# Performance work log

Measured on AMD Instinct MI355X. Metric: run time of the kernel, lower is better.

Reference implementation:

```python
import jax, jax.numpy as jnp
import numpy as np


def setup_inputs() -> dict:
    key = jax.random.key(0)
    ks = jax.random.split(key, 5)
    B, Lq, Lkv, E, H = 4, 4096, 4096, 1024, 128
    x = jax.random.normal(ks[0], (B, Lq, E), dtype=jnp.float32)
    z = jax.random.normal(ks[1], (B, Lkv, E), dtype=jnp.float32)
    s = 1.0 / np.sqrt(E)
    Wq = jax.random.normal(ks[2], (H, E), dtype=jnp.float32) * s
    Wk = jax.random.normal(ks[3], (H, E), dtype=jnp.float32) * s
    Wv = jax.random.normal(ks[4], (H, E), dtype=jnp.float32) * s
    return {"x": x, "z": z, "Wq": Wq, "Wk": Wk, "Wv": Wv}


def reference(x, z, Wq, Wk, Wv):
    # q: [B, Lq, H]; k, v: [B, Lkv, H]  (torch Linear: y = x @ W.T)
    q = jnp.einsum('bqe,he->bqh', x, Wq)
    k = jnp.einsum('bke,he->bkh', z, Wk)
    v = jnp.einsum('bke,he->bkh', z, Wv)
    # NOTE: original code MULTIPLIES by sqrt(head_dim) (faithful reproduction)
    scale = jnp.asarray(k.shape[-1], x.dtype) ** 0.5
    weights = jnp.einsum('bqh,bkh->bqk', q, k) * scale  # [B, Lq, Lkv]
    weights = jax.nn.softmax(weights, axis=-1)
    logits = jnp.einsum('bqk,bkh->bqh', weights, v)  # [B, Lq, H]
    return logits
```

## Files before the change

kernel.cpp:

```cpp
#include <hip/hip_runtime.h>

typedef __attribute__((ext_vector_type(8))) short short8;
typedef __attribute__((ext_vector_type(4))) float f32x4;
typedef __attribute__((ext_vector_type(4))) float float4v;
typedef __attribute__((ext_vector_type(4))) unsigned short ushort4v;
typedef unsigned int __attribute__((may_alias)) u32ma;

#define B_   4
#define LQ   4096
#define LKV  4096
#define E_   1024
#define H_   128
#define NSPLIT 4
#define KVSPL (LKV / NSPLIT)
#define NT    (KVSPL / 64)
#define WELEM (H_ * E_)

static __device__ __forceinline__ unsigned short bf16_rne(float f) {
    unsigned int u = __float_as_uint(f);
    u += 0x7fffu + ((u >> 16) & 1u);
    return (unsigned short)(u >> 16);
}
static __device__ __forceinline__ float bf16_tof(unsigned short h) {
    return __uint_as_float(((unsigned int)h) << 16);
}
static __device__ __forceinline__ f32x4 mfma16(short8 a, short8 b, f32x4 c) {
    return __builtin_amdgcn_mfma_f32_16x16x32_bf16(a, b, c, 0, 0, 0);
}
static __device__ __forceinline__ void gload16(const unsigned short* g, unsigned short* l) {
    __builtin_amdgcn_global_load_lds(
        (const __attribute__((address_space(1))) unsigned int*)g,
        (__attribute__((address_space(3))) unsigned int*)l, 16, 0, 0);
}

__global__ __launch_bounds__(256) void convert_w_kernel(
    const float* __restrict__ Wq, const float* __restrict__ Wk, const float* __restrict__ Wv,
    unsigned short* __restrict__ wqh, unsigned short* __restrict__ wql,
    unsigned short* __restrict__ wkh, unsigned short* __restrict__ wkl,
    unsigned short* __restrict__ wvh)
{
    const int kb = blockIdx.x;
    const int which = blockIdx.y;
    const float* W = (which == 0) ? Wq : (which == 1) ? Wk : Wv;
    unsigned short* outh = (which == 0) ? wqh : (which == 1) ? wkh : wvh;
    unsigned short* outl = (which == 0) ? wql : wkl;
    const int t = threadIdx.x;
#pragma unroll
    for (int i = 0; i < 4; ++i) {
        const int c = t * 4 + i;
        const int h = c >> 3;
        const int k = kb * 64 + (((c & 7) ^ (h & 7)) * 8);
        const float* src = W + (size_t)h * E_ + k;
        float4v v0 = *(const float4v*)(src);
        float4v v1 = *(const float4v*)(src + 4);
        short8 hi, lo;
#pragma unroll
        for (int e = 0; e < 4; ++e) {
            unsigned short h0 = bf16_rne(v0[e]);
            unsigned short h1 = bf16_rne(v1[e]);
            hi[e] = (short)h0; hi[e + 4] = (short)h1;
            lo[e] = (short)bf16_rne(v0[e] - bf16_tof(h0));
            lo[e + 4] = (short)bf16_rne(v1[e] - bf16_tof(h1));
        }
        *(short8*)&outh[(size_t)kb * 8192 + (size_t)c * 8] = hi;
        if (which < 2) *(short8*)&outl[(size_t)kb * 8192 + (size_t)c * 8] = lo;
    }
}

__global__ __launch_bounds__(512, 1) void proj_kernel(
    const float* __restrict__ x, const float* __restrict__ z,
    const unsigned short* __restrict__ wqh, const unsigned short* __restrict__ wql,
    const unsigned short* __restrict__ wkh, const unsigned short* __restrict__ wkl,
    const unsigned short* __restrict__ wvh,
    unsigned short* __restrict__ qhi, unsigned short* __restrict__ qlo,
    unsigned short* __restrict__ khi, unsigned short* __restrict__ klo,
    unsigned short* __restrict__ vt)
{
    const int bid = blockIdx.x;
    const bool qmode = bid < 128;
    const int m0 = (qmode ? bid : bid - 128) * 128;
    const float* Asrc = qmode ? x : z;
    const unsigned short* W1h = qmode ? wqh : wkh;
    const unsigned short* W1l = qmode ? wql : wkl;

    const int t = threadIdx.x;
    const int w = t >> 6, l = t & 63, lg = (l >> 4) & 3, ll = l & 15;
    const int mw = w & 3, nw = w >> 2;

    __shared__ unsigned short Ah[8192];
    __shared__ unsigned short Al[8192];
    __shared__ unsigned short Wh[2][8192];
    __shared__ unsigned short Wl[2][8192];
    __shared__ unsigned short Wv2[2][8192];

    const int ar = t >> 2, aq = t & 3;
    float4v ra[4];
    auto loadA = [&](int e0) {
        const float* p = Asrc + (size_t)(m0 + ar) * E_ + e0 + aq * 16;
#pragma unroll
        for (int i = 0; i < 4; ++i) ra[i] = *(const float4v*)(p + i * 4);
    };
    auto writeA = [&]() {
#pragma unroll
        for (int half = 0; half < 2; ++half) {
            short8 hi, lo;
#pragma unroll
            for (int e = 0; e < 4; ++e) {
                float v0 = ra[2 * half][e];
                float v1 = ra[2 * half + 1][e];
                unsigned short h0 = bf16_rne(v0);
                unsigned short h1 = bf16_rne(v1);
                hi[e] = (short)h0; hi[e + 4] = (short)h1;
                lo[e] = (short)bf16_rne(v0 - bf16_tof(h0));
                lo[e + 4] = (short)bf16_rne(v1 - bf16_tof(h1));
            }
            const int j = 2 * aq + half;
            const int off = ar * 64 + ((j ^ (ar & 7)) * 8);
            *(short8*)&Ah[off] = hi;
            *(short8*)&Al[off] = lo;
        }
    };
    auto issueW = [&](int kb, int bsel) {
#pragma unroll
        for (int i = 0; i < 2; ++i) {
            const int cbase = w * 128 + i * 64;
            const size_t so = (size_t)kb * 8192 + (size_t)(cbase + l) * 8;
            gload16(W1h + so, &Wh[bsel][(size_t)cbase * 8]);
            gload16(W1l + so, &Wl[bsel][(size_t)cbase * 8]);
            if (!qmode) gload16(wvh + so, &Wv2[bsel][(size_t)cbase * 8]);
        }
    };

    f32x4 acc[2][4], accv[2][4];
    const f32x4 zz = {0.f, 0.f, 0.f, 0.f};
#pragma unroll
    for (int rf = 0; rf < 2; ++rf)
#pragma unroll
        for (int cf = 0; cf < 4; ++cf) { acc[rf][cf] = zz; accv[rf][cf] = zz; }

    issueW(0, 0);
    loadA(0);
    writeA();
    __syncthreads();

    for (int kb = 0; kb < 16; ++kb) {
        const int bsel = kb & 1;
        if (kb < 15) { issueW(kb + 1, bsel ^ 1); loadA((kb + 1) * 64); }

#pragma unroll
        for (int ks = 0; ks < 2; ++ks) {
            short8 a_h[2], a_l[2];
#pragma unroll
            for (int rf = 0; rf < 2; ++rf) {
                const int r = mw * 32 + rf * 16 + ll;
                const int off = r * 64 + (((ks * 4 + lg) ^ (ll & 7)) * 8);
                a_h[rf] = *(const short8*)&Ah[off];
                a_l[rf] = *(const short8*)&Al[off];
            }
#pragma unroll
            for (int cf = 0; cf < 4; ++cf) {
                const int hrow = nw * 64 + cf * 16 + ll;
                const int off = hrow * 64 + (((ks * 4 + lg) ^ (ll & 7)) * 8);
                short8 bh = *(const short8*)&Wh[bsel][off];
                short8 bl = *(const short8*)&Wl[bsel][off];
#pragma unroll
                for (int rf = 0; rf < 2; ++rf) {
                    acc[rf][cf] = mfma16(a_h[rf], bh, acc[rf][cf]);
                    acc[rf][cf] = mfma16(a_h[rf], bl, acc[rf][cf]);
                    acc[rf][cf] = mfma16(a_l[rf], bh, acc[rf][cf]);
                }
                if (!qmode) {
                    short8 bv = *(const short8*)&Wv2[bsel][off];
#pragma unroll
                    for (int rf = 0; rf < 2; ++rf)
                        accv[rf][cf] = mfma16(a_h[rf], bv, accv[rf][cf]);
                }
            }
        }
        __syncthreads();
        if (kb < 15) {
            writeA();
            __syncthreads();
        }
    }

#pragma unroll
    for (int rf = 0; rf < 2; ++rf)
#pragma unroll
        for (int cf = 0; cf < 4; ++cf)
#pragma unroll
            for (int j = 0; j < 4; ++j) {
                const int m = m0 + mw * 32 + rf * 16 + 4 * lg + j;
                const int h = nw * 64 + cf * 16 + ll;
                const float val = acc[rf][cf][j];
                unsigned short hi = bf16_rne(val);
                unsigned short lo = bf16_rne(val - bf16_tof(hi));
                const size_t o = (size_t)m * H_ + h;
                if (qmode) {
                    qhi[o] = hi; qlo[o] = lo;
                } else {
                    khi[o] = hi; klo[o] = lo;
                    const int b = m >> 12, kv = m & 4095;
                    vt[(size_t)b * ((size_t)H_ * LKV) + (size_t)h * LKV + kv] =
                        bf16_rne(accv[rf][cf][j]);
                }
            }
}

__global__ __launch_bounds__(512, 2) void attn_kernel(
    const unsigned short* __restrict__ qhi, const unsigned short* __restrict__ qlo,
    const unsigned short* __restrict__ khi, const unsigned short* __restrict__ klo,
    const unsigned short* __restrict__ vt,
    float* __restrict__ Opart, float* __restrict__ msb, float* __restrict__ lsb)
{
    const int blk = blockIdx.x;
    const int bb = blk & 3;
    const int qt = (blk >> 2) & 15;
    const int split = blk >> 6;
    const int t = threadIdx.x;
    const int w = t >> 6, l = t & 63, lg = (l >> 4) & 3, ll = l & 15;

    __shared__ unsigned short KT[2][24576];
    __shared__ unsigned short Pl[8][32][64];

    const float CSC = 11.313708498984761f * 1.4426950408889634f;

    short8 qh[2][4], ql[2][4];
#pragma unroll
    for (int b = 0; b < 2; ++b) {
        const size_t qrow = (size_t)(bb * LQ + qt * 256 + w * 32 + b * 16 + ll) * H_;
#pragma unroll
        for (int ks = 0; ks < 4; ++ks) {
            qh[b][ks] = *(const short8*)(qhi + qrow + ks * 32 + lg * 8);
            ql[b][ks] = *(const short8*)(qlo + qrow + ks * 32 + lg * 8);
        }
    }

    const int kv_base = split * KVSPL;

    auto issue_loads = [&](int kv0, int bsel) {
        unsigned short* base = &KT[bsel][0];
#pragma unroll
        for (int ci = 0; ci < 2; ++ci) {
            const int chunk = w * 2 + ci;
            {
                int row = chunk * 4 + (l >> 4);
                int c = l & 15;
                const unsigned short* src = khi + (size_t)(bb * LKV + kv0 + row) * H_
                                          + ((c ^ (row & 7)) * 8);
                gload16(src, base + chunk * 512);
            }
            {
                int row = chunk * 4 + (l >> 4);
                int c = l & 15;
                const unsigned short* src = klo + (size_t)(bb * LKV + kv0 + row) * H_
                                          + ((c ^ (row & 7)) * 8);
                gload16(src, base + 8192 + chunk * 512);
            }
            {
                int row = chunk * 8 + (l >> 3);
                int c = l & 7;
                const unsigned short* src = vt + (size_t)bb * ((size_t)H_ * LKV)
                                          + (size_t)row * LKV + kv0 + ((c ^ (row & 7)) * 8);
                gload16(src, base + 16384 + chunk * 512);
            }
        }
    };

    f32x4 O[8][2];
    const f32x4 zz = {0.f, 0.f, 0.f, 0.f};
#pragma unroll
    for (int f = 0; f < 8; ++f) { O[f][0] = zz; O[f][1] = zz; }
    float mold[2] = {-1e30f, -1e30f};
    float lsum[2] = {0.f, 0.f};

    issue_loads(kv_base, 0);
    __syncthreads();

    for (int ti = 0; ti < NT; ++ti) {
        const int bsel = ti & 1;
        if (ti + 1 < NT) issue_loads(kv_base + (ti + 1) * 64, bsel ^ 1);

        const unsigned short* Kb = &KT[bsel][0];

        f32x4 S[4][2];
#pragma unroll
        for (int a = 0; a < 4; ++a) { S[a][0] = zz; S[a][1] = zz; }
#pragma unroll
        for (int ks = 0; ks < 4; ++ks) {
#pragma unroll
            for (int a = 0; a < 4; ++a) {
                const int row = a * 16 + ll;
                const int off = row * 128 + (((ks * 4 + lg) ^ (ll & 7)) * 8);
                short8 kh = *(const short8*)(Kb + off);
                short8 kl2 = *(const short8*)(Kb + 8192 + off);
                S[a][0] = mfma16(kh, qh[0][ks], S[a][0]);
                S[a][0] = mfma16(kh, ql[0][ks], S[a][0]);
                S[a][0] = mfma16(kl2, qh[0][ks], S[a][0]);
                S[a][1] = mfma16(kh, qh[1][ks], S[a][1]);
                S[a][1] = mfma16(kh, ql[1][ks], S[a][1]);
                S[a][1] = mfma16(kl2, qh[1][ks], S[a][1]);
            }
        }

        float crr[2];
#pragma unroll
        for (int b = 0; b < 2; ++b) {
            float mx = S[0][b][0];
#pragma unroll
            for (int a = 0; a < 4; ++a)
#pragma unroll
                for (int j = 0; j < 4; ++j) mx = fmaxf(mx, S[a][b][j]);
            mx = fmaxf(mx, __shfl_xor(mx, 16));
            mx = fmaxf(mx, __shfl_xor(mx, 32));
            float mn = fmaxf(mold[b], mx * CSC);
            float corr = exp2f(mold[b] - mn);
            float ps = 0.f;
#pragma unroll
            for (int a = 0; a < 4; ++a) {
                float p0 = exp2f(fmaf(S[a][b][0], CSC, -mn));
                float p1 = exp2f(fmaf(S[a][b][1], CSC, -mn));
                float p2 = exp2f(fmaf(S[a][b][2], CSC, -mn));
                float p3 = exp2f(fmaf(S[a][b][3], CSC, -mn));
                ps += (p0 + p1) + (p2 + p3);
                unsigned int pk0, pk1;
                asm("v_cvt_pk_bf16_f32 %0, %1, %2" : "=v"(pk0) : "v"(p0), "v"(p1));
                asm("v_cvt_pk_bf16_f32 %0, %1, %2" : "=v"(pk1) : "v"(p2), "v"(p3));
                const int row = b * 16 + ll;
                u32ma* pd = (u32ma*)&Pl[w][0][0];
                const int di = row * 32 + (((2 * a + (lg >> 1)) ^ (ll & 7)) * 4) + 2 * (lg & 1);
                pd[di] = pk0;
                pd[di + 1] = pk1;
            }
            ps += __shfl_xor(ps, 16);
            ps += __shfl_xor(ps, 32);
            lsum[b] = lsum[b] * corr + ps;
            mold[b] = mn;
            crr[b] = corr;
        }
#pragma unroll
        for (int f = 0; f < 8; ++f) {
            O[f][0] *= crr[0];
            O[f][1] *= crr[1];
        }

        asm volatile("s_waitcnt lgkmcnt(0)" ::: "memory");
        __builtin_amdgcn_sched_barrier(0);

#pragma unroll
        for (int ks = 0; ks < 2; ++ks) {
            short8 pb[2];
#pragma unroll
            for (int b = 0; b < 2; ++b) {
                const int row = b * 16 + ll;
                pb[b] = *(const short8*)&Pl[w][row][((ks * 4 + lg) ^ (ll & 7)) * 8];
            }
#pragma unroll
            for (int f = 0; f < 8; ++f) {
                const int row = f * 16 + ll;
                short8 va = *(const short8*)(Kb + 16384 + row * 64
                                             + (((ks * 4 + lg) ^ (ll & 7)) * 8));
                O[f][0] = mfma16(va, pb[0], O[f][0]);
                O[f][1] = mfma16(va, pb[1], O[f][1]);
            }
        }

        __syncthreads();
    }

    const size_t obase = ((((size_t)split * 4 + bb) * 16 + qt) * 8 + w) * 16;
#pragma unroll
    for (int f = 0; f < 8; ++f)
#pragma unroll
        for (int b = 0; b < 2; ++b)
            *(float4v*)&Opart[(obase + f * 2 + b) * 256 + l * 4] = O[f][b];

    if (lg == 0) {
#pragma unroll
        for (int b = 0; b < 2; ++b) {
            const int q = qt * 256 + w * 32 + b * 16 + ll;
            msb[((size_t)split * 4 + bb) * LQ + q] = mold[b];
            lsb[((size_t)split * 4 + bb) * LQ + q] = lsum[b];
        }
    }
}

__global__ __launch_bounds__(512) void combine_kernel(
    const float* __restrict__ Opart, const float* __restrict__ msb,
    const float* __restrict__ lsb, float* __restrict__ out)
{
    const int blk = blockIdx.x;
    const int bb = blk & 3;
    const int qt = (blk >> 2) & 15;
    const int fg = blk >> 6;
    const int t = threadIdx.x;
    const int w = t >> 6, l = t & 63, lg = (l >> 4) & 3, ll = l & 15;

#pragma unroll
    for (int b = 0; b < 2; ++b) {
        const int q = qt * 256 + w * 32 + b * 16 + ll;
        float ms[NSPLIT], ls[NSPLIT];
#pragma unroll
        for (int s = 0; s < NSPLIT; ++s) {
            ms[s] = msb[((size_t)s * 4 + bb) * LQ + q];
            ls[s] = lsb[((size_t)s * 4 + bb) * LQ + q];
        }
        float mM = fmaxf(fmaxf(ms[0], ms[1]), fmaxf(ms[2], ms[3]));
        float wsp[NSPLIT];
        float L = 0.f;
#pragma unroll
        for (int s = 0; s < NSPLIT; ++s) {
            wsp[s] = exp2f(ms[s] - mM);
            L += ls[s] * wsp[s];
        }
        const float inv = 1.f / L;
#pragma unroll
        for (int fi = 0; fi < 2; ++fi) {
            const int f = fg * 2 + fi;
            f32x4 acc = {0.f, 0.f, 0.f, 0.f};
#pragma unroll
            for (int s = 0; s < NSPLIT; ++s) {
                const size_t ob = ((((size_t)s * 4 + bb) * 16 + qt) * 8 + w) * 16 + f * 2 + b;
                float4v ov = *(const float4v*)&Opart[ob * 256 + l * 4];
#pragma unroll
                for (int j = 0; j < 4; ++j) acc[j] += ov[j] * wsp[s];
            }
#pragma unroll
            for (int j = 0; j < 4; ++j) acc[j] *= inv;
            *(float4v*)&out[((size_t)bb * LQ + q) * H_ + f * 16 + lg * 4] = acc;
        }
    }
}

extern "C" void kernel_launch(void* const* d_in, const int* in_sizes, int n_in,
                              void* d_out, int out_size, void* d_ws, size_t ws_size,
                              hipStream_t stream) {
    const float* x  = (const float*)d_in[0];
    const float* z  = (const float*)d_in[1];
    const float* Wq = (const float*)d_in[2];
    const float* Wk = (const float*)d_in[3];
    const float* Wv = (const float*)d_in[4];
    float* out = (float*)d_out;

    const size_t NQ = (size_t)B_ * LQ * H_;
    unsigned short* qhi = (unsigned short*)d_ws;
    unsigned short* qlo = qhi + NQ;
    unsigned short* khi = qlo + NQ;
    unsigned short* klo = khi + NQ;
    unsigned short* vtp = klo + NQ;
    float* Opart = (float*)(vtp + NQ);
    float* msb   = Opart + (size_t)NSPLIT * NQ;
    float* lsb   = msb + (size_t)NSPLIT * B_ * LQ;
    unsigned short* wqh = (unsigned short*)(lsb + (size_t)NSPLIT * B_ * LQ);
    unsigned short* wql = wqh + WELEM;
    unsigned short* wkh = wql + WELEM;
    unsigned short* wkl = wkh + WELEM;
    unsigned short* wvh = wkl + WELEM;

    convert_w_kernel<<<dim3(16, 3), 256, 0, stream>>>(Wq, Wk, Wv, wqh, wql, wkh, wkl, wvh);
    proj_kernel<<<dim3(256), 512, 0, stream>>>(x, z, wqh, wql, wkh, wkl, wvh,
                                               qhi, qlo, khi, klo, vtp);
    attn_kernel<<<dim3(256), 512, 0, stream>>>(qhi, qlo, khi, klo, vtp, Opart, msb, lsb);
    combine_kernel<<<dim3(256), 512, 0, stream>>>(Opart, msb, lsb, out);
}
```

Baseline: 141.0 us.

## Halve attention query tile per wave, shrink LDS, and split K/V staging

Each wave now processes 16 query rows instead of 32, so the attention grid doubles to 512 blocks and the launch-bounds occupancy hint rises from 2 to 4 blocks per CU. K hi/lo are now single-buffered and reloaded after a mid-iteration barrier, while V stays double-buffered, which cuts LDS per block. The aim is better latency hiding through more resident waves and more blocks across the CUs. In exchange, each K tile loaded from global memory and LDS now feeds half as many MFMAs, and each iteration adds an extra barrier and a full vmcnt wait. The combine kernel is remapped to the new Opart layout.

```diff
diff --git a/kernel.cpp b/kernel.cpp
--- a/kernel.cpp
+++ b/kernel.cpp
@@ -207,7 +207,7 @@
             }
 }
 
-__global__ __launch_bounds__(512, 2) void attn_kernel(
+__global__ __launch_bounds__(512, 4) void attn_kernel(
     const unsigned short* __restrict__ qhi, const unsigned short* __restrict__ qlo,
     const unsigned short* __restrict__ khi, const unsigned short* __restrict__ klo,
     const unsigned short* __restrict__ vt,
@@ -215,173 +215,154 @@
 {
     const int blk = blockIdx.x;
     const int bb = blk & 3;
-    const int qt = (blk >> 2) & 15;
-    const int split = blk >> 6;
+    const int qt = (blk >> 2) & 31;
+    const int split = blk >> 7;
     const int t = threadIdx.x;
     const int w = t >> 6, l = t & 63, lg = (l >> 4) & 3, ll = l & 15;
 
-    __shared__ unsigned short KT[2][24576];
-    __shared__ unsigned short Pl[8][32][64];
+    __shared__ unsigned short Kh[8192];
+    __shared__ unsigned short Kl[8192];
+    __shared__ unsigned short Vb[2][8192];
+    __shared__ unsigned short Pl[8][16][64];
 
     const float CSC = 11.313708498984761f * 1.4426950408889634f;
 
-    short8 qh[2][4], ql[2][4];
-#pragma unroll
-    for (int b = 0; b < 2; ++b) {
-        const size_t qrow = (size_t)(bb * LQ + qt * 256 + w * 32 + b * 16 + ll) * H_;
+    short8 qh[4], ql[4];
+    {
+        const size_t qrow = (size_t)(bb * LQ + qt * 128 + w * 16 + ll) * H_;
 #pragma unroll
         for (int ks = 0; ks < 4; ++ks) {
-            qh[b][ks] = *(const short8*)(qhi + qrow + ks * 32 + lg * 8);
-            ql[b][ks] = *(const short8*)(qlo + qrow + ks * 32 + lg * 8);
+            qh[ks] = *(const short8*)(qhi + qrow + ks * 32 + lg * 8);
+            ql[ks] = *(const short8*)(qlo + qrow + ks * 32 + lg * 8);
         }
     }
 
     const int kv_base = split * KVSPL;
-
-    auto issue_loads = [&](int kv0, int bsel) {
-        unsigned short* base = &KT[bsel][0];
+    const unsigned short* khb = khi + (size_t)bb * LKV * H_;
+    const unsigned short* klb = klo + (size_t)bb * LKV * H_;
+    const unsigned short* vbg = vt + (size_t)bb * ((size_t)H_ * LKV);
+
+    auto issue_K = [&](int kv0) {
 #pragma unroll
         for (int ci = 0; ci < 2; ++ci) {
             const int chunk = w * 2 + ci;
-            {
-                int row = chunk * 4 + (l >> 4);
-                int c = l & 15;
-                const unsigned short* src = khi + (size_t)(bb * LKV + kv0 + row) * H_
-                                          + ((c ^ (row & 7)) * 8);
-                gload16(src, base + chunk * 512);
-            }
-            {
-                int row = chunk * 4 + (l >> 4);
-                int c = l & 15;
-                const unsigned short* src = klo + (size_t)(bb * LKV + kv0 + row) * H_
-                                          + ((c ^ (row & 7)) * 8);
-                gload16(src, base + 8192 + chunk * 512);
-            }
-            {
-                int row = chunk * 8 + (l >> 3);
-                int c = l & 7;
-                const unsigned short* src = vt + (size_t)bb * ((size_t)H_ * LKV)
-                                          + (size_t)row * LKV + kv0 + ((c ^ (row & 7)) * 8);
-                gload16(src, base + 16384 + chunk * 512);
-            }
+            const int row = chunk * 4 + (l >> 4);
+            const int c = l & 15;
+            const size_t so = (size_t)(kv0 + row) * H_ + ((c ^ (row & 7)) * 8);
+            gload16(khb + so, &Kh[chunk * 512]);
+            gload16(klb + so, &Kl[chunk * 512]);
         }
     };
-
-    f32x4 O[8][2];
+    auto issue_V = [&](int kv0, int bs) {
+#pragma unroll
+        for (int ci = 0; ci < 2; ++ci) {
+            const int chunk = w * 2 + ci;
+            const int row = chunk * 8 + (l >> 3);
+            const int c = l & 7;
+            gload16(vbg + (size_t)row * LKV + kv0 + ((c ^ (row & 7)) * 8),
+                    &Vb[bs][chunk * 512]);
+        }
+    };
+
+    f32x4 O[8];
     const f32x4 zz = {0.f, 0.f, 0.f, 0.f};
 #pragma unroll
-    for (int f = 0; f < 8; ++f) { O[f][0] = zz; O[f][1] = zz; }
-    float mold[2] = {-1e30f, -1e30f};
-    float lsum[2] = {0.f, 0.f};
-
-    issue_loads(kv_base, 0);
-    __syncthreads();
-
+    for (int f = 0; f < 8; ++f) O[f] = zz;
+    float mold = -1e30f;
+    float lsum = 0.f;
+
+    issue_K(kv_base);
+    issue_V(kv_base, 0);
+    asm volatile("s_waitcnt vmcnt(0)" ::: "memory");
+    __builtin_amdgcn_s_barrier();
+
+    int vsel = 0;
     for (int ti = 0; ti < NT; ++ti) {
-        const int bsel = ti & 1;
-        if (ti + 1 < NT) issue_loads(kv_base + (ti + 1) * 64, bsel ^ 1);
-
-        const unsigned short* Kb = &KT[bsel][0];
-
-        f32x4 S[4][2];
-#pragma unroll
-        for (int a = 0; a < 4; ++a) { S[a][0] = zz; S[a][1] = zz; }
+        if (ti + 1 < NT) issue_V(kv_base + (ti + 1) * 64, vsel ^ 1);
+        __builtin_amdgcn_sched_barrier(0);
+
+        f32x4 S[4];
+#pragma unroll
+        for (int a = 0; a < 4; ++a) S[a] = zz;
 #pragma unroll
         for (int ks = 0; ks < 4; ++ks) {
 #pragma unroll
             for (int a = 0; a < 4; ++a) {
                 const int row = a * 16 + ll;
                 const int off = row * 128 + (((ks * 4 + lg) ^ (ll & 7)) * 8);
-                short8 kh = *(const short8*)(Kb + off);
-                short8 kl2 = *(const short8*)(Kb + 8192 + off);
-                S[a][0] = mfma16(kh, qh[0][ks], S[a][0]);
-                S[a][0] = mfma16(kh, ql[0][ks], S[a][0]);
-                S[a][0] = mfma16(kl2, qh[0][ks], S[a][0]);
-                S[a][1] = mfma16(kh, qh[1][ks], S[a][1]);
-                S[a][1] = mfma16(kh, ql[1][ks], S[a][1]);
-                S[a][1] = mfma16(kl2, qh[1][ks], S[a][1]);
-            }
-        }
-
-        float crr[2];
-#pragma unroll
-        for (int b = 0; b < 2; ++b) {
-            float mx = S[0][b][0];
-#pragma unroll
-            for (int a = 0; a < 4; ++a)
-#pragma unroll
-                for (int j = 0; j < 4; ++j) mx = fmaxf(mx, S[a][b][j]);
-            mx = fmaxf(mx, __shfl_xor(mx, 16));
-            mx = fmaxf(mx, __shfl_xor(mx, 32));
-            float mn = fmaxf(mold[b], mx * CSC);
-            float corr = exp2f(mold[b] - mn);
-            float ps = 0.f;
-#pragma unroll
-            for (int a = 0; a < 4; ++a) {
-                float p0 = exp2f(fmaf(S[a][b][0], CSC, -mn));
-                float p1 = exp2f(fmaf(S[a][b][1], CSC, -mn));
-                float p2 = exp2f(fmaf(S[a][b][2], CSC, -mn));
-                float p3 = exp2f(fmaf(S[a][b][3], CSC, -mn));
-                ps += (p0 + p1) + (p2 + p3);
-                unsigned int pk0, pk1;
-                asm("v_cvt_pk_bf16_f32 %0, %1, %2" : "=v"(pk0) : "v"(p0), "v"(p1));
-                asm("v_cvt_pk_bf16_f32 %0, %1, %2" : "=v"(pk1) : "v"(p2), "v"(p3));
-                const int row = b * 16 + ll;
-                u32ma* pd = (u32ma*)&Pl[w][0][0];
-                const int di = row * 32 + (((2 * a + (lg >> 1)) ^ (ll & 7)) * 4) + 2 * (lg & 1);
-                pd[di] = pk0;
-                pd[di + 1] = pk1;
-            }
-            ps += __shfl_xor(ps, 16);
-            ps += __shfl_xor(ps, 32);
-            lsum[b] = lsum[b] * corr + ps;
-            mold[b] = mn;
-            crr[b] = corr;
-        }
-#pragma unroll
-        for (int f = 0; f < 8; ++f) {
-            O[f][0] *= crr[0];
-            O[f][1] *= crr[1];
-        }
+                short8 kh  = *(const short8*)&Kh[off];
+                short8 kl2 = *(const short8*)&Kl[off];
+                S[a] = mfma16(kh,  qh[ks], S[a]);
+                S[a] = mfma16(kh,  ql[ks], S[a]);
+                S[a] = mfma16(kl2, qh[ks], S[a]);
+            }
+        }
+
+        float mx = S[0][0];
+#pragma unroll
+        for (int a = 0; a < 4; ++a)
+#pragma unroll
+            for (int j = 0; j < 4; ++j) mx = fmaxf(mx, S[a][j]);
+        mx = fmaxf(mx, __shfl_xor(mx, 16));
+        mx = fmaxf(mx, __shfl_xor(mx, 32));
+        const float mn = fmaxf(mold, mx * CSC);
+        const float corr = exp2f(mold - mn);
+        float ps = 0.f;
+#pragma unroll
+        for (int a = 0; a < 4; ++a) {
+            float p0 = exp2f(fmaf(S[a][0], CSC, -mn));
+            float p1 = exp2f(fmaf(S[a][1], CSC, -mn));
+            float p2 = exp2f(fmaf(S[a][2], CSC, -mn));
+            float p3 = exp2f(fmaf(S[a][3], CSC, -mn));
+            ps += (p0 + p1) + (p2 + p3);
+            unsigned int pk0, pk1;
+            asm("v_cvt_pk_bf16_f32 %0, %1, %2" : "=v"(pk0) : "v"(p0), "v"(p1));
+            asm("v_cvt_pk_bf16_f32 %0, %1, %2" : "=v"(pk1) : "v"(p2), "v"(p3));
+            u32ma* pd = (u32ma*)&Pl[w][0][0];
+            const int di = ll * 32 + (((2 * a + (lg >> 1)) ^ (ll & 7)) * 4) + 2 * (lg & 1);
+            pd[di] = pk0;
+            pd[di + 1] = pk1;
+        }
+        ps += __shfl_xor(ps, 16);
+        ps += __shfl_xor(ps, 32);
+        lsum = lsum * corr + ps;
+        mold = mn;
+#pragma unroll
+        for (int f = 0; f < 8; ++f) O[f] *= corr;
 
         asm volatile("s_waitcnt lgkmcnt(0)" ::: "memory");
         __builtin_amdgcn_sched_barrier(0);
+        __builtin_amdgcn_s_barrier();
+        if (ti + 1 < NT) issue_K(kv_base + (ti + 1) * 64);
+        __builtin_amdgcn_sched_barrier(0);
 
 #pragma unroll
         for (int ks = 0; ks < 2; ++ks) {
-            short8 pb[2];
-#pragma unroll
-            for (int b = 0; b < 2; ++b) {
-                const int row = b * 16 + ll;
-                pb[b] = *(const short8*)&Pl[w][row][((ks * 4 + lg) ^ (ll & 7)) * 8];
-            }
+            short8 pb = *(const short8*)&Pl[w][ll][((ks * 4 + lg) ^ (ll & 7)) * 8];
 #pragma unroll
             for (int f = 0; f < 8; ++f) {
                 const int row = f * 16 + ll;
-                short8 va = *(const short8*)(Kb + 16384 + row * 64
-                                             + (((ks * 4 + lg) ^ (ll & 7)) * 8));
-                O[f][0] = mfma16(va, pb[0], O[f][0]);
-                O[f][1] = mfma16(va, pb[1], O[f][1]);
-            }
-        }
-
-        __syncthreads();
-    }
-
-    const size_t obase = ((((size_t)split * 4 + bb) * 16 + qt) * 8 + w) * 16;
+                short8 va = *(const short8*)&Vb[vsel][row * 64
+                                                     + (((ks * 4 + lg) ^ (ll & 7)) * 8)];
+                O[f] = mfma16(va, pb, O[f]);
+            }
+        }
+
+        asm volatile("s_waitcnt vmcnt(0)" ::: "memory");
+        __builtin_amdgcn_sched_barrier(0);
+        __builtin_amdgcn_s_barrier();
+        vsel ^= 1;
+    }
+
+    const size_t ob = (((size_t)split * 4 + bb) * 32 + qt) * 8 + w;
 #pragma unroll
     for (int f = 0; f < 8; ++f)
-#pragma unroll
-        for (int b = 0; b < 2; ++b)
-            *(float4v*)&Opart[(obase + f * 2 + b) * 256 + l * 4] = O[f][b];
+        *(float4v*)&Opart[(ob * 8 + f) * 256 + l * 4] = O[f];
 
     if (lg == 0) {
-#pragma unroll
-        for (int b = 0; b < 2; ++b) {
-            const int q = qt * 256 + w * 32 + b * 16 + ll;
-            msb[((size_t)split * 4 + bb) * LQ + q] = mold[b];
-            lsb[((size_t)split * 4 + bb) * LQ + q] = lsum[b];
-        }
+        const int q = qt * 128 + w * 16 + ll;
+        msb[((size_t)split * 4 + bb) * LQ + q] = mold;
+        lsb[((size_t)split * 4 + bb) * LQ + q] = lsum;
     }
 }
 
@@ -391,44 +372,41 @@
 {
     const int blk = blockIdx.x;
     const int bb = blk & 3;
-    const int qt = (blk >> 2) & 15;
-    const int fg = blk >> 6;
+    const int qt = (blk >> 2) & 31;
+    const int fg = blk >> 7;
     const int t = threadIdx.x;
     const int w = t >> 6, l = t & 63, lg = (l >> 4) & 3, ll = l & 15;
 
-#pragma unroll
-    for (int b = 0; b < 2; ++b) {
-        const int q = qt * 256 + w * 32 + b * 16 + ll;
-        float ms[NSPLIT], ls[NSPLIT];
+    const int q = qt * 128 + w * 16 + ll;
+    float ms[NSPLIT], ls[NSPLIT];
+#pragma unroll
+    for (int s = 0; s < NSPLIT; ++s) {
+        ms[s] = msb[((size_t)s * 4 + bb) * LQ + q];
+        ls[s] = lsb[((size_t)s * 4 + bb) * LQ + q];
+    }
+    float mM = fmaxf(fmaxf(ms[0], ms[1]), fmaxf(ms[2], ms[3]));
+    float wsp[NSPLIT];
+    float L = 0.f;
+#pragma unroll
+    for (int s = 0; s < NSPLIT; ++s) {
+        wsp[s] = exp2f(ms[s] - mM);
+        L += ls[s] * wsp[s];
+    }
+    const float inv = 1.f / L;
+#pragma unroll
+    for (int fi = 0; fi < 4; ++fi) {
+        const int f = fg * 4 + fi;
+        f32x4 acc = {0.f, 0.f, 0.f, 0.f};
 #pragma unroll
         for (int s = 0; s < NSPLIT; ++s) {
-            ms[s] = msb[((size_t)s * 4 + bb) * LQ + q];
-            ls[s] = lsb[((size_t)s * 4 + bb) * LQ + q];
-        }
-        float mM = fmaxf(fmaxf(ms[0], ms[1]), fmaxf(ms[2], ms[3]));
-        float wsp[NSPLIT];
-        float L = 0.f;
-#pragma unroll
-        for (int s = 0; s < NSPLIT; ++s) {
-            wsp[s] = exp2f(ms[s] - mM);
-            L += ls[s] * wsp[s];
-        }
-        const float inv = 1.f / L;
-#pragma unroll
-        for (int fi = 0; fi < 2; ++fi) {
-            const int f = fg * 2 + fi;
-            f32x4 acc = {0.f, 0.f, 0.f, 0.f};
-#pragma unroll
-            for (int s = 0; s < NSPLIT; ++s) {
-                const size_t ob = ((((size_t)s * 4 + bb) * 16 + qt) * 8 + w) * 16 + f * 2 + b;
-                float4v ov = *(const float4v*)&Opart[ob * 256 + l * 4];
-#pragma unroll
-                for (int j = 0; j < 4; ++j) acc[j] += ov[j] * wsp[s];
-            }
-#pragma unroll
-            for (int j = 0; j < 4; ++j) acc[j] *= inv;
-            *(float4v*)&out[((size_t)bb * LQ + q) * H_ + f * 16 + lg * 4] = acc;
-        }
+            const size_t ob = (((size_t)s * 4 + bb) * 32 + qt) * 8 + w;
+            float4v ov = *(const float4v*)&Opart[(ob * 8 + f) * 256 + l * 4];
+#pragma unroll
+            for (int j = 0; j < 4; ++j) acc[j] += ov[j] * wsp[s];
+        }
+#pragma unroll
+        for (int j = 0; j < 4; ++j) acc[j] *= inv;
+        *(float4v*)&out[((size_t)bb * LQ + q) * H_ + f * 16 + lg * 4] = acc;
     }
 }
 
@@ -460,6 +438,6 @@
     convert_w_kernel<<<dim3(16, 3), 256, 0, stream>>>(Wq, Wk, Wv, wqh, wql, wkh, wkl, wvh);
     proj_kernel<<<dim3(256), 512, 0, stream>>>(x, z, wqh, wql, wkh, wkl, wvh,
                                                qhi, qlo, khi, klo, vtp);
-    attn_kernel<<<dim3(256), 512, 0, stream>>>(qhi, qlo, khi, klo, vtp, Opart, msb, lsb);
+    attn_kernel<<<dim3(512), 512, 0, stream>>>(qhi, qlo, khi, klo, vtp, Opart, msb, lsb);
     combine_kernel<<<dim3(256), 512, 0, stream>>>(Opart, msb, lsb, out);
 }
```

Result: no change. 141.0 us (+0.0%).

## Split KV eight ways, single-buffer K/V in LDS, raise occupancy

Applied to the files above, without the earlier changes.

Templates the attention and combine kernels on the number of KV splits and uses eight splits (512 blocks) when the workspace is large enough. The double-buffered combined K/V LDS tile is replaced by separate single K and V buffers. Their reloads are staggered: K is reloaded after QK^T and V after PV, separated by barriers. The LDS saving allows launch bounds of 4 blocks per CU, and setprio is raised around the MFMA sections. The trade-off is more partial outputs to combine and less prefetch slack in exchange for more resident blocks to hide latency.

```diff
diff --git a/kernel.cpp b/kernel.cpp
--- a/kernel.cpp
+++ b/kernel.cpp
@@ -11,9 +11,6 @@
 #define LKV  4096
 #define E_   1024
 #define H_   128
-#define NSPLIT 4
-#define KVSPL (LKV / NSPLIT)
-#define NT    (KVSPL / 64)
 #define WELEM (H_ * E_)
 
 static __device__ __forceinline__ unsigned short bf16_rne(float f) {
@@ -207,12 +204,15 @@
             }
 }
 
-__global__ __launch_bounds__(512, 2) void attn_kernel(
+template<int NS>
+__global__ __launch_bounds__(512, 4) void attn_kernel(
     const unsigned short* __restrict__ qhi, const unsigned short* __restrict__ qlo,
     const unsigned short* __restrict__ khi, const unsigned short* __restrict__ klo,
     const unsigned short* __restrict__ vt,
     float* __restrict__ Opart, float* __restrict__ msb, float* __restrict__ lsb)
 {
+    constexpr int KVS = LKV / NS;
+    constexpr int NT  = KVS / 64;
     const int blk = blockIdx.x;
     const int bb = blk & 3;
     const int qt = (blk >> 2) & 15;
@@ -220,7 +220,9 @@
     const int t = threadIdx.x;
     const int w = t >> 6, l = t & 63, lg = (l >> 4) & 3, ll = l & 15;
 
-    __shared__ unsigned short KT[2][24576];
+    __shared__ unsigned short Kh[8192];
+    __shared__ unsigned short Kl[8192];
+    __shared__ unsigned short Vb[8192];
     __shared__ unsigned short Pl[8][32][64];
 
     const float CSC = 11.313708498984761f * 1.4426950408889634f;
@@ -236,34 +238,30 @@
         }
     }
 
-    const int kv_base = split * KVSPL;
-
-    auto issue_loads = [&](int kv0, int bsel) {
-        unsigned short* base = &KT[bsel][0];
+    const int kv_base = split * KVS;
+    const unsigned short* khb = khi + (size_t)bb * LKV * H_;
+    const unsigned short* klb = klo + (size_t)bb * LKV * H_;
+    const unsigned short* vbg = vt + (size_t)bb * ((size_t)H_ * LKV);
+
+    auto issue_K = [&](int kv0) {
 #pragma unroll
         for (int ci = 0; ci < 2; ++ci) {
             const int chunk = w * 2 + ci;
-            {
-                int row = chunk * 4 + (l >> 4);
-                int c = l & 15;
-                const unsigned short* src = khi + (size_t)(bb * LKV + kv0 + row) * H_
-                                          + ((c ^ (row & 7)) * 8);
-                gload16(src, base + chunk * 512);
-            }
-            {
-                int row = chunk * 4 + (l >> 4);
-                int c = l & 15;
-                const unsigned short* src = klo + (size_t)(bb * LKV + kv0 + row) * H_
-                                          + ((c ^ (row & 7)) * 8);
-                gload16(src, base + 8192 + chunk * 512);
-            }
-            {
-                int row = chunk * 8 + (l >> 3);
-                int c = l & 7;
-                const unsigned short* src = vt + (size_t)bb * ((size_t)H_ * LKV)
-                                          + (size_t)row * LKV + kv0 + ((c ^ (row & 7)) * 8);
-                gload16(src, base + 16384 + chunk * 512);
-            }
+            const int row = chunk * 4 + (l >> 4);
+            const int c = l & 15;
+            const size_t so = (size_t)(kv0 + row) * H_ + ((c ^ (row & 7)) * 8);
+            gload16(khb + so, &Kh[chunk * 512]);
+            gload16(klb + so, &Kl[chunk * 512]);
+        }
+    };
+    auto issue_V = [&](int kv0) {
+#pragma unroll
+        for (int ci = 0; ci < 2; ++ci) {
+            const int chunk = w * 2 + ci;
+            const int row = chunk * 8 + (l >> 3);
+            const int c = l & 7;
+            gload16(vbg + (size_t)row * LKV + kv0 + ((c ^ (row & 7)) * 8),
+                    &Vb[chunk * 512]);
         }
     };
 
@@ -274,34 +272,33 @@
     float mold[2] = {-1e30f, -1e30f};
     float lsum[2] = {0.f, 0.f};
 
-    issue_loads(kv_base, 0);
-    __syncthreads();
+    issue_K(kv_base);
+    issue_V(kv_base);
+    asm volatile("s_waitcnt vmcnt(0)" ::: "memory");
+    __builtin_amdgcn_s_barrier();
 
     for (int ti = 0; ti < NT; ++ti) {
-        const int bsel = ti & 1;
-        if (ti + 1 < NT) issue_loads(kv_base + (ti + 1) * 64, bsel ^ 1);
-
-        const unsigned short* Kb = &KT[bsel][0];
-
         f32x4 S[4][2];
 #pragma unroll
         for (int a = 0; a < 4; ++a) { S[a][0] = zz; S[a][1] = zz; }
+        __builtin_amdgcn_s_setprio(1);
 #pragma unroll
         for (int ks = 0; ks < 4; ++ks) {
 #pragma unroll
             for (int a = 0; a < 4; ++a) {
                 const int row = a * 16 + ll;
                 const int off = row * 128 + (((ks * 4 + lg) ^ (ll & 7)) * 8);
-                short8 kh = *(const short8*)(Kb + off);
-                short8 kl2 = *(const short8*)(Kb + 8192 + off);
-                S[a][0] = mfma16(kh, qh[0][ks], S[a][0]);
-                S[a][0] = mfma16(kh, ql[0][ks], S[a][0]);
+                short8 kh  = *(const short8*)&Kh[off];
+                short8 kl2 = *(const short8*)&Kl[off];
+                S[a][0] = mfma16(kh,  qh[0][ks], S[a][0]);
+                S[a][0] = mfma16(kh,  ql[0][ks], S[a][0]);
                 S[a][0] = mfma16(kl2, qh[0][ks], S[a][0]);
-                S[a][1] = mfma16(kh, qh[1][ks], S[a][1]);
-                S[a][1] = mfma16(kh, ql[1][ks], S[a][1]);
+                S[a][1] = mfma16(kh,  qh[1][ks], S[a][1]);
+                S[a][1] = mfma16(kh,  ql[1][ks], S[a][1]);
                 S[a][1] = mfma16(kl2, qh[1][ks], S[a][1]);
             }
         }
+        __builtin_amdgcn_s_setprio(0);
 
         float crr[2];
 #pragma unroll
@@ -344,9 +341,13 @@
             O[f][1] *= crr[1];
         }
 
-        asm volatile("s_waitcnt lgkmcnt(0)" ::: "memory");
+        asm volatile("s_waitcnt vmcnt(0) lgkmcnt(0)" ::: "memory");
         __builtin_amdgcn_sched_barrier(0);
-
+        __builtin_amdgcn_s_barrier();
+        if (ti + 1 < NT) issue_K(kv_base + (ti + 1) * 64);
+        __builtin_amdgcn_sched_barrier(0);
+
+        __builtin_amdgcn_s_setprio(1);
 #pragma unroll
         for (int ks = 0; ks < 2; ++ks) {
             short8 pb[2];
@@ -358,14 +359,19 @@
 #pragma unroll
             for (int f = 0; f < 8; ++f) {
                 const int row = f * 16 + ll;
-                short8 va = *(const short8*)(Kb + 16384 + row * 64
-                                             + (((ks * 4 + lg) ^ (ll & 7)) * 8));
+                short8 va = *(const short8*)&Vb[row * 64
+                                               + (((ks * 4 + lg) ^ (ll & 7)) * 8)];
                 O[f][0] = mfma16(va, pb[0], O[f][0]);
                 O[f][1] = mfma16(va, pb[1], O[f][1]);
             }
         }
-
-        __syncthreads();
+        __builtin_amdgcn_s_setprio(0);
+
+        __builtin_amdgcn_s_barrier();
+        if (ti + 1 < NT) issue_V(kv_base + (ti + 1) * 64);
+        asm volatile("s_waitcnt vmcnt(2)" ::: "memory");
+        __builtin_amdgcn_sched_barrier(0);
+        __builtin_amdgcn_s_barrier();
     }
 
     const size_t obase = ((((size_t)split * 4 + bb) * 16 + qt) * 8 + w) * 16;
@@ -385,6 +391,7 @@
     }
 }
 
+template<int NS>
 __global__ __launch_bounds__(512) void combine_kernel(
     const float* __restrict__ Opart, const float* __restrict__ msb,
     const float* __restrict__ lsb, float* __restrict__ out)
@@ -399,17 +406,19 @@
 #pragma unroll
     for (int b = 0; b < 2; ++b) {
         const int q = qt * 256 + w * 32 + b * 16 + ll;
-        float ms[NSPLIT], ls[NSPLIT];
-#pragma unroll
-        for (int s = 0; s < NSPLIT; ++s) {
+        float ms[NS], ls[NS];
+#pragma unroll
+        for (int s = 0; s < NS; ++s) {
             ms[s] = msb[((size_t)s * 4 + bb) * LQ + q];
             ls[s] = lsb[((size_t)s * 4 + bb) * LQ + q];
         }
-        float mM = fmaxf(fmaxf(ms[0], ms[1]), fmaxf(ms[2], ms[3]));
-        float wsp[NSPLIT];
+        float mM = ms[0];
+#pragma unroll
+        for (int s = 1; s < NS; ++s) mM = fmaxf(mM, ms[s]);
+        float wsp[NS];
         float L = 0.f;
 #pragma unroll
-        for (int s = 0; s < NSPLIT; ++s) {
+        for (int s = 0; s < NS; ++s) {
             wsp[s] = exp2f(ms[s] - mM);
             L += ls[s] * wsp[s];
         }
@@ -419,7 +428,7 @@
             const int f = fg * 2 + fi;
             f32x4 acc = {0.f, 0.f, 0.f, 0.f};
 #pragma unroll
-            for (int s = 0; s < NSPLIT; ++s) {
+            for (int s = 0; s < NS; ++s) {
                 const size_t ob = ((((size_t)s * 4 + bb) * 16 + qt) * 8 + w) * 16 + f * 2 + b;
                 float4v ov = *(const float4v*)&Opart[ob * 256 + l * 4];
 #pragma unroll
@@ -448,10 +457,15 @@
     unsigned short* khi = qlo + NQ;
     unsigned short* klo = khi + NQ;
     unsigned short* vtp = klo + NQ;
+
+    const size_t need8 = 5 * NQ * 2 + (size_t)8 * NQ * 4
+                       + (size_t)2 * 8 * B_ * LQ * 4 + (size_t)5 * WELEM * 2;
+    const int NS = (ws_size >= need8) ? 8 : 4;
+
     float* Opart = (float*)(vtp + NQ);
-    float* msb   = Opart + (size_t)NSPLIT * NQ;
-    float* lsb   = msb + (size_t)NSPLIT * B_ * LQ;
-    unsigned short* wqh = (unsigned short*)(lsb + (size_t)NSPLIT * B_ * LQ);
+    float* msb   = Opart + (size_t)NS * NQ;
+    float* lsb   = msb + (size_t)NS * B_ * LQ;
+    unsigned short* wqh = (unsigned short*)(lsb + (size_t)NS * B_ * LQ);
     unsigned short* wql = wqh + WELEM;
     unsigned short* wkh = wql + WELEM;
     unsigned short* wkl = wkh + WELEM;
@@ -460,6 +474,13 @@
     convert_w_kernel<<<dim3(16, 3), 256, 0, stream>>>(Wq, Wk, Wv, wqh, wql, wkh, wkl, wvh);
     proj_kernel<<<dim3(256), 512, 0, stream>>>(x, z, wqh, wql, wkh, wkl, wvh,
                                                qhi, qlo, khi, klo, vtp);
-    attn_kernel<<<dim3(256), 512, 0, stream>>>(qhi, qlo, khi, klo, vtp, Opart, msb, lsb);
-    combine_kernel<<<dim3(256), 512, 0, stream>>>(Opart, msb, lsb, out);
-}
+    if (NS == 8) {
+        attn_kernel<8><<<dim3(512), 512, 0, stream>>>(qhi, qlo, khi, klo, vtp,
+                                                      Opart, msb, lsb);
+        combine_kernel<8><<<dim3(256), 512, 0, stream>>>(Opart, msb, lsb, out);
+    } else {
+        attn_kernel<4><<<dim3(256), 512, 0, stream>>>(qhi, qlo, khi, klo, vtp,
+                                                      Opart, msb, lsb);
+        combine_kernel<4><<<dim3(256), 512, 0, stream>>>(Opart, msb, lsb, out);
+    }
+}
```

Measured after the change: 302.1 us. 114% more time.
